# Kernel optimization log

Hardware: AMD Instinct MI355X
Metric: run time of the kernel (lower is better)

## Reference

```python
import jax, jax.numpy as jnp
import numpy as np

BITS = 4
MAXQ = 15          # (1 << BITS) - 1
PACK = 32 // BITS  # 8 values packed per int32


def dequantize(qweight, qzeros, scales, g_idx):
    """GPTQ 4-bit dequant. qweight: [K//8, N] int32, qzeros: [G, N//8] int32,
    scales: [G, N] float, g_idx: [K] int32 -> dense W [K, N] float."""
    N = qweight.shape[1]
    shifts = (jnp.arange(PACK, dtype=jnp.uint32) * BITS)  # [8]
    qw = qweight.astype(jnp.uint32)
    # unpack along K: k = row*8 + j  (matches shifter = (k % 8) * bits)
    w_int = ((qw[:, None, :] >> shifts[None, :, None]) & MAXQ).reshape(-1, N)  # [K, N]
    qz = qzeros.astype(jnp.uint32)
    # unpack along N: n = col*8 + j  (matches zeros_shifter = (n % 8) * bits)
    z_int = ((qz[:, :, None] >> shifts[None, None, :]) & MAXQ).reshape(qzeros.shape[0], -1) + 1  # [G, N]
    dt = scales.dtype
    # group-wise dequant: w = (q - zero) * scale, gathered per-row via g_idx
    return (w_int.astype(dt) - z_int[g_idx].astype(dt)) * scales[g_idx]


def setup_inputs() -> dict:
    key = jax.random.key(0)
    k1, k2, k3, k4, k5 = jax.random.split(key, 5)
    M, K, N, GS = 128, 4096, 11008, 128
    G = K // GS
    x = jax.random.normal(k1, (M, K), dtype=jnp.float32)
    qweight = jax.random.randint(k2, (K // PACK, N), 0, 2147483647, dtype=jnp.int32)
    qzeros = jax.random.randint(k3, (G, N // PACK), 0, 2147483647, dtype=jnp.int32)
    scales = jax.random.uniform(k4, (G, N), dtype=jnp.float32, minval=0.001, maxval=0.01)
    bias = jax.random.normal(k5, (N,), dtype=jnp.float32)
    g_idx = (jnp.arange(K, dtype=jnp.int32) // GS).astype(jnp.int32)
    return {"x": x, "qweight": qweight, "qzeros": qzeros, "scales": scales,
            "bias": bias, "g_idx": g_idx}


def reference(x, qweight, qzeros, scales, bias, g_idx):
    w = dequantize(qweight, qzeros, scales, g_idx)  # [K, N]
    return x @ w + bias
```

## Files before the change

kernel.cpp:

```cpp
#include <hip/hip_runtime.h>
#include <stdint.h>


#define M_DIM 128
#define K_DIM 4096
#define N_DIM 11008
#define GS    128
#define NG    32
#define SPLIT 4
#define GPB   (NG / SPLIT)
#define PART_STRIDE ((size_t)M_DIM * N_DIM)

typedef _Float16 half8  __attribute__((ext_vector_type(8)));
typedef _Float16 half2t __attribute__((ext_vector_type(2)));
typedef _Float16 half4t __attribute__((ext_vector_type(4)));
typedef float    f32x4  __attribute__((ext_vector_type(4)));

__global__ void k_prep(const float* __restrict__ x, const int* __restrict__ qzeros,
                       const float* __restrict__ scales,
                       _Float16* __restrict__ xh, half2t* __restrict__ zsc) {
    int b = blockIdx.x, tid = threadIdx.x;
    if (b < 512) {
        int i = (b * 256 + tid) * 4;
        float4 v = *(const float4*)(x + i);
        half4t o;
        o[0] = (_Float16)v.x; o[1] = (_Float16)v.y;
        o[2] = (_Float16)v.z; o[3] = (_Float16)v.w;
        *(half4t*)(xh + i) = o;
    } else {
        b -= 512;
        int g = b / 43;
        int n = (b - g * 43) * 256 + tid;
        unsigned qz = (unsigned)qzeros[g * (N_DIM / 8) + (n >> 3)];
        float z1 = (float)((qz >> ((n & 7) * 4)) & 15u) + 1.0f;
        float s  = scales[g * N_DIM + n];
        half2t o;
        o[0] = (_Float16)s;
        o[1] = (_Float16)(-z1 * s);
        zsc[g * N_DIM + n] = o;
    }
}

__device__ __forceinline__ void load_lds16(const void* g, void* l) {
    __builtin_amdgcn_global_load_lds(
        (const __attribute__((address_space(1))) unsigned int*)g,
        (__attribute__((address_space(3))) unsigned int*)l, 16, 0, 0);
}

__device__ __forceinline__ half8 dequant8(unsigned q, half2t S2, half2t Z2) {
    const half2t BIAS = __builtin_bit_cast(half2t, 0x64006400u);
    half2t w[4];
#pragma unroll
    for (int p = 0; p < 4; ++p) {
        unsigned r = __builtin_amdgcn_perm(q, q, 0x00010001u * (unsigned)p);
        unsigned t = (r & 0x00F0000Fu) | 0x64006400u;
        w[p] = __builtin_elementwise_fma(__builtin_bit_cast(half2t, t) - BIAS, S2, Z2);
    }
    half4t lo = __builtin_shufflevector(w[0], w[1], 0, 1, 2, 3);
    half4t hi = __builtin_shufflevector(w[2], w[3], 0, 1, 2, 3);
    return __builtin_shufflevector(lo, hi, 0, 1, 2, 3, 4, 5, 6, 7);
}

__global__ __launch_bounds__(512, 4)
void k_gemm(const _Float16* __restrict__ xh,
            const int*      __restrict__ qweight,
            const half2t*   __restrict__ zsc,
            float*          __restrict__ part)
{
    __shared__ _Float16 As[2][128 * 128];

    const int tid  = threadIdx.x;
    const int lane = tid & 63;
    const int w    = tid >> 6;
    const int wx   = w & 1;
    const int wy   = (w >> 1) & 1;
    const int kh   = w >> 2;
    const int q    = lane >> 4;
    const int lr   = lane & 15;

    const int n0 = blockIdx.x * 64;
    const int g0 = blockIdx.y * GPB;
    int ncol[2] = { n0 + wx * 32 + lr, n0 + wx * 32 + lr + 16 };

    f32x4 acc[4][2];
#pragma unroll
    for (int f = 0; f < 4; ++f)
#pragma unroll
        for (int h = 0; h < 2; ++h)
            acc[f][h] = (f32x4){0.f, 0.f, 0.f, 0.f};

    int cm[4], ckb[4];
#pragma unroll
    for (int it = 0; it < 4; ++it) {
        int c = it * 512 + tid;
        cm[it]  = c >> 4;
        ckb[it] = (c & 15) ^ (cm[it] & 15);
    }
    const int wave_lds = w * 64 * 8;

#pragma unroll
    for (int it = 0; it < 4; ++it)
        load_lds16(xh + (size_t)cm[it] * K_DIM + g0 * GS + ckb[it] * 8,
                   &As[0][it * 512 * 8 + wave_lds]);

    unsigned qwA[GPB][4];
    half2t   zs2[GPB][2];
#pragma unroll
    for (int gg = 0; gg < GPB; ++gg) {
        int ga = g0 + gg;
#pragma unroll
        for (int t = 0; t < 2; ++t)
#pragma unroll
            for (int h = 0; h < 2; ++h)
                qwA[gg][t * 2 + h] =
                    (unsigned)qweight[(size_t)(ga * 16 + (kh * 2 + t) * 4 + q) * N_DIM + ncol[h]];
#pragma unroll
        for (int h = 0; h < 2; ++h)
            zs2[gg][h] = zsc[(size_t)ga * N_DIM + ncol[h]];
    }

#pragma unroll
    for (int g = 0; g < GPB; ++g) {
        __syncthreads();

        if (g + 1 < GPB) {
            int gn = g0 + g + 1;
#pragma unroll
            for (int it = 0; it < 4; ++it)
                load_lds16(xh + (size_t)cm[it] * K_DIM + gn * GS + ckb[it] * 8,
                           &As[(g + 1) & 1][it * 512 * 8 + wave_lds]);
        }

        const half2t SC = { (_Float16)1.0f, (_Float16)0.0625f };
        half2t S2[2], Z2[2];
#pragma unroll
        for (int h = 0; h < 2; ++h) {
            half2t ss = __builtin_shufflevector(zs2[g][h], zs2[g][h], 0, 0);
            S2[h] = ss * SC;
            Z2[h] = __builtin_shufflevector(zs2[g][h], zs2[g][h], 1, 1);
        }

#pragma unroll
        for (int t = 0; t < 2; ++t) {
            const int kk = kh * 2 + t;
            half8 bf[2];
#pragma unroll
            for (int h = 0; h < 2; ++h)
                bf[h] = dequant8(qwA[g][t * 2 + h], S2[h], Z2[h]);
#pragma unroll
            for (int f = 0; f < 4; ++f) {
                int m   = wy * 64 + f * 16 + lr;
                int kb2 = (kk * 4 + q) ^ lr;
                half8 af = *(const half8*)(&As[g & 1][m * 128 + kb2 * 8]);
#pragma unroll
                for (int h = 0; h < 2; ++h)
                    acc[f][h] = __builtin_amdgcn_mfma_f32_16x16x32_f16(af, bf[h], acc[f][h], 0, 0, 0);
            }
        }
    }

    __syncthreads();
    float* red = (float*)&As[0][0];
    const int pid = w & 3;
    if (w >= 4) {
#pragma unroll
        for (int f = 0; f < 4; ++f)
#pragma unroll
            for (int h = 0; h < 2; ++h)
                *(f32x4*)(red + pid * 2048 + (f * 2 + h) * 256 + lane * 4) = acc[f][h];
    }
    __syncthreads();
    if (w < 4) {
        float* po = part + (size_t)blockIdx.y * PART_STRIDE;
#pragma unroll
        for (int f = 0; f < 4; ++f) {
            int mrow = wy * 64 + f * 16 + q * 4;
#pragma unroll
            for (int h = 0; h < 2; ++h) {
                f32x4 o = acc[f][h] + *(const f32x4*)(red + pid * 2048 + (f * 2 + h) * 256 + lane * 4);
#pragma unroll
                for (int r = 0; r < 4; ++r)
                    po[(size_t)(mrow + r) * N_DIM + ncol[h]] = o[r];
            }
        }
    }
}

__global__ void k_reduce(const float* __restrict__ part, const float* __restrict__ bias,
                         float* __restrict__ out) {
    int i = (blockIdx.x * 256 + threadIdx.x) * 4;
    int m = i / N_DIM;
    int n = i - m * N_DIM;
    f32x4 s = *(const f32x4*)(bias + n);
#pragma unroll
    for (int sp = 0; sp < SPLIT; ++sp)
        s += *(const f32x4*)(part + sp * PART_STRIDE + i);
    *(f32x4*)(out + i) = s;
}

extern "C" void kernel_launch(void* const* d_in, const int* in_sizes, int n_in,
                              void* d_out, int out_size, void* d_ws, size_t ws_size,
                              hipStream_t stream) {
    const float* x       = (const float*)d_in[0];
    const int*   qweight = (const int*)d_in[1];
    const int*   qzeros  = (const int*)d_in[2];
    const float* scales  = (const float*)d_in[3];
    const float* bias    = (const float*)d_in[4];

    char* ws = (char*)d_ws;
    _Float16* xh   = (_Float16*)ws;
    half2t*   zsc  = (half2t*)(ws + 1048576);
    float*    part = (float*)(ws + 1048576 + 1409024);

    k_prep  <<<dim3(1888),            dim3(256), 0, stream>>>(x, qzeros, scales, xh, zsc);
    k_gemm  <<<dim3(N_DIM/64, SPLIT), dim3(512), 0, stream>>>(xh, qweight, zsc, part);
    k_reduce<<<dim3(1376),            dim3(256), 0, stream>>>(part, bias, (float*)d_out);
}
```

Before: 105.2 us.

## Replace split-K with M-split tiling and fuse bias into GEMM epilogue

Replaces the split-K decomposition, which wrote four fp32 partial outputs and needed a separate reduce kernel, with full-K accumulation per block. The block now covers 64 rows of M, using a 256-wide K tile with a register-prefetched weight pipeline. Bias is added in the epilogue and the reduce launch plus the partial-buffer traffic are removed. The trade-off is that each weight tile is now read and dequantized twice, once per M half, and each block runs a longer serial K loop (16 iterations) with less per-block MFMA reuse of the dequantized B fragments.

```diff
diff --git a/kernel.cpp b/kernel.cpp
--- a/kernel.cpp
+++ b/kernel.cpp
@@ -6,10 +6,8 @@
 #define K_DIM 4096
 #define N_DIM 11008
 #define GS    128
-#define NG    32
-#define SPLIT 4
-#define GPB   (NG / SPLIT)
-#define PART_STRIDE ((size_t)M_DIM * N_DIM)
+#define BK    256
+#define NITER (K_DIM / BK)
 
 typedef _Float16 half8  __attribute__((ext_vector_type(8)));
 typedef _Float16 half2t __attribute__((ext_vector_type(2)));
@@ -65,9 +63,10 @@
 void k_gemm(const _Float16* __restrict__ xh,
             const int*      __restrict__ qweight,
             const half2t*   __restrict__ zsc,
-            float*          __restrict__ part)
+            const float*    __restrict__ bias,
+            float*          __restrict__ out)
 {
-    __shared__ _Float16 As[2][128 * 128];
+    __shared__ _Float16 As[2][64 * 256];
 
     const int tid  = threadIdx.x;
     const int lane = tid & 63;
@@ -79,12 +78,12 @@
     const int lr   = lane & 15;
 
     const int n0 = blockIdx.x * 64;
-    const int g0 = blockIdx.y * GPB;
+    const int m0 = blockIdx.y * 64;
     int ncol[2] = { n0 + wx * 32 + lr, n0 + wx * 32 + lr + 16 };
 
-    f32x4 acc[4][2];
-#pragma unroll
-    for (int f = 0; f < 4; ++f)
+    f32x4 acc[2][2];
+#pragma unroll
+    for (int f = 0; f < 2; ++f)
 #pragma unroll
         for (int h = 0; h < 2; ++h)
             acc[f][h] = (f32x4){0.f, 0.f, 0.f, 0.f};
@@ -93,65 +92,75 @@
 #pragma unroll
     for (int it = 0; it < 4; ++it) {
         int c = it * 512 + tid;
-        cm[it]  = c >> 4;
-        ckb[it] = (c & 15) ^ (cm[it] & 15);
-    }
-    const int wave_lds = w * 64 * 8;
+        cm[it] = c >> 5;
+        int j  = c & 31;
+        ckb[it] = (j & 16) | ((j & 15) ^ (cm[it] & 15));
+    }
+    const int wave_lds = w * 512;
 
 #pragma unroll
     for (int it = 0; it < 4; ++it)
-        load_lds16(xh + (size_t)cm[it] * K_DIM + g0 * GS + ckb[it] * 8,
-                   &As[0][it * 512 * 8 + wave_lds]);
-
-    unsigned qwA[GPB][4];
-    half2t   zs2[GPB][2];
-#pragma unroll
-    for (int gg = 0; gg < GPB; ++gg) {
-        int ga = g0 + gg;
-#pragma unroll
-        for (int t = 0; t < 2; ++t)
+        load_lds16(xh + (size_t)(m0 + cm[it]) * K_DIM + ckb[it] * 8,
+                   &As[0][it * 4096 + wave_lds]);
+    unsigned qwn[8];
+    half2t   zsn[2];
+#pragma unroll
+    for (int t = 0; t < 4; ++t)
+#pragma unroll
+        for (int h = 0; h < 2; ++h)
+            qwn[t * 2 + h] = (unsigned)qweight[(size_t)((kh * 4 + t) * 4 + q) * N_DIM + ncol[h]];
+#pragma unroll
+    for (int h = 0; h < 2; ++h) zsn[h] = zsc[(size_t)kh * N_DIM + ncol[h]];
+    float bv[2] = { bias[ncol[0]], bias[ncol[1]] };
+
+#pragma unroll 2
+    for (int i = 0; i < NITER; ++i) {
+        unsigned qw[8];
+        half2t   zs[2];
+#pragma unroll
+        for (int j = 0; j < 8; ++j) qw[j] = qwn[j];
+#pragma unroll
+        for (int h = 0; h < 2; ++h) zs[h] = zsn[h];
+
+        __syncthreads();
+
+        if (i + 1 < NITER) {
+#pragma unroll
+            for (int it = 0; it < 4; ++it)
+                load_lds16(xh + (size_t)(m0 + cm[it]) * K_DIM + (i + 1) * BK + ckb[it] * 8,
+                           &As[(i + 1) & 1][it * 4096 + wave_lds]);
+#pragma unroll
+            for (int t = 0; t < 4; ++t)
+#pragma unroll
+                for (int h = 0; h < 2; ++h)
+                    qwn[t * 2 + h] = (unsigned)qweight[(size_t)((i + 1) * 32 + (kh * 4 + t) * 4 + q) * N_DIM + ncol[h]];
 #pragma unroll
             for (int h = 0; h < 2; ++h)
-                qwA[gg][t * 2 + h] =
-                    (unsigned)qweight[(size_t)(ga * 16 + (kh * 2 + t) * 4 + q) * N_DIM + ncol[h]];
-#pragma unroll
-        for (int h = 0; h < 2; ++h)
-            zs2[gg][h] = zsc[(size_t)ga * N_DIM + ncol[h]];
-    }
-
-#pragma unroll
-    for (int g = 0; g < GPB; ++g) {
-        __syncthreads();
-
-        if (g + 1 < GPB) {
-            int gn = g0 + g + 1;
-#pragma unroll
-            for (int it = 0; it < 4; ++it)
-                load_lds16(xh + (size_t)cm[it] * K_DIM + gn * GS + ckb[it] * 8,
-                           &As[(g + 1) & 1][it * 512 * 8 + wave_lds]);
+                zsn[h] = zsc[(size_t)(2 * (i + 1) + kh) * N_DIM + ncol[h]];
         }
 
         const half2t SC = { (_Float16)1.0f, (_Float16)0.0625f };
         half2t S2[2], Z2[2];
 #pragma unroll
         for (int h = 0; h < 2; ++h) {
-            half2t ss = __builtin_shufflevector(zs2[g][h], zs2[g][h], 0, 0);
+            half2t ss = __builtin_shufflevector(zs[h], zs[h], 0, 0);
             S2[h] = ss * SC;
-            Z2[h] = __builtin_shufflevector(zs2[g][h], zs2[g][h], 1, 1);
-        }
-
-#pragma unroll
-        for (int t = 0; t < 2; ++t) {
-            const int kk = kh * 2 + t;
+            Z2[h] = __builtin_shufflevector(zs[h], zs[h], 1, 1);
+        }
+
+#pragma unroll
+        for (int t = 0; t < 4; ++t) {
+            const int kk = kh * 4 + t;
             half8 bf[2];
 #pragma unroll
             for (int h = 0; h < 2; ++h)
-                bf[h] = dequant8(qwA[g][t * 2 + h], S2[h], Z2[h]);
-#pragma unroll
-            for (int f = 0; f < 4; ++f) {
-                int m   = wy * 64 + f * 16 + lr;
-                int kb2 = (kk * 4 + q) ^ lr;
-                half8 af = *(const half8*)(&As[g & 1][m * 128 + kb2 * 8]);
+                bf[h] = dequant8(qw[t * 2 + h], S2[h], Z2[h]);
+#pragma unroll
+            for (int f = 0; f < 2; ++f) {
+                int m    = wy * 32 + f * 16 + lr;
+                int kb2  = kk * 4 + q;
+                int phys = (kb2 & 16) | ((kb2 & 15) ^ lr);
+                half8 af = *(const half8*)(&As[i & 1][m * 256 + phys * 8]);
 #pragma unroll
                 for (int h = 0; h < 2; ++h)
                     acc[f][h] = __builtin_amdgcn_mfma_f32_16x16x32_f16(af, bf[h], acc[f][h], 0, 0, 0);
@@ -162,40 +171,27 @@
     __syncthreads();
     float* red = (float*)&As[0][0];
     const int pid = w & 3;
-    if (w >= 4) {
-#pragma unroll
-        for (int f = 0; f < 4; ++f)
+    if (kh == 1) {
+#pragma unroll
+        for (int f = 0; f < 2; ++f)
 #pragma unroll
             for (int h = 0; h < 2; ++h)
                 *(f32x4*)(red + pid * 2048 + (f * 2 + h) * 256 + lane * 4) = acc[f][h];
     }
     __syncthreads();
-    if (w < 4) {
-        float* po = part + (size_t)blockIdx.y * PART_STRIDE;
-#pragma unroll
-        for (int f = 0; f < 4; ++f) {
-            int mrow = wy * 64 + f * 16 + q * 4;
+    if (kh == 0) {
+#pragma unroll
+        for (int f = 0; f < 2; ++f) {
+            int mrow = m0 + wy * 32 + f * 16 + q * 4;
 #pragma unroll
             for (int h = 0; h < 2; ++h) {
                 f32x4 o = acc[f][h] + *(const f32x4*)(red + pid * 2048 + (f * 2 + h) * 256 + lane * 4);
 #pragma unroll
                 for (int r = 0; r < 4; ++r)
-                    po[(size_t)(mrow + r) * N_DIM + ncol[h]] = o[r];
+                    out[(size_t)(mrow + r) * N_DIM + ncol[h]] = o[r] + bv[h];
             }
         }
     }
-}
-
-__global__ void k_reduce(const float* __restrict__ part, const float* __restrict__ bias,
-                         float* __restrict__ out) {
-    int i = (blockIdx.x * 256 + threadIdx.x) * 4;
-    int m = i / N_DIM;
-    int n = i - m * N_DIM;
-    f32x4 s = *(const f32x4*)(bias + n);
-#pragma unroll
-    for (int sp = 0; sp < SPLIT; ++sp)
-        s += *(const f32x4*)(part + sp * PART_STRIDE + i);
-    *(f32x4*)(out + i) = s;
 }
 
 extern "C" void kernel_launch(void* const* d_in, const int* in_sizes, int n_in,
@@ -208,11 +204,9 @@
     const float* bias    = (const float*)d_in[4];
 
     char* ws = (char*)d_ws;
-    _Float16* xh   = (_Float16*)ws;
-    half2t*   zsc  = (half2t*)(ws + 1048576);
-    float*    part = (float*)(ws + 1048576 + 1409024);
-
-    k_prep  <<<dim3(1888),            dim3(256), 0, stream>>>(x, qzeros, scales, xh, zsc);
-    k_gemm  <<<dim3(N_DIM/64, SPLIT), dim3(512), 0, stream>>>(xh, qweight, zsc, part);
-    k_reduce<<<dim3(1376),            dim3(256), 0, stream>>>(part, bias, (float*)d_out);
-}
+    _Float16* xh  = (_Float16*)ws;
+    half2t*   zsc = (half2t*)(ws + 1048576);
+
+    k_prep<<<dim3(1888),    dim3(256), 0, stream>>>(x, qzeros, scales, xh, zsc);
+    k_gemm<<<dim3(172, 2),  dim3(512), 0, stream>>>(xh, qweight, zsc, bias, (float*)d_out);
+}
```

After: 112.7 us. 7.1% more time.

## Pre-swizzle activations into MFMA fragment layout and drop LDS staging

Applied to the files above, without the earlier changes.

The prep kernel now writes the fp16 activations already arranged in per-lane MFMA A-fragment order. The GEMM kernel can then load A fragments straight from global memory with register double-buffering instead of staging tiles through LDS with barriers. Blocks shrink to 256 threads, and each wave owns 32 rows across the full 64 columns and the whole split-K range, which removes the in-block LDS reduction. The cost is that A fragments are re-read from global/L2 by every block, with no LDS reuse across waves, and weight loads are pipelined one step ahead rather than fully prefetched.

```diff
diff --git a/kernel.cpp b/kernel.cpp
--- a/kernel.cpp
+++ b/kernel.cpp
@@ -6,31 +6,39 @@
 #define K_DIM 4096
 #define N_DIM 11008
 #define GS    128
-#define NG    32
 #define SPLIT 4
-#define GPB   (NG / SPLIT)
+#define STEPS 32
 #define PART_STRIDE ((size_t)M_DIM * N_DIM)
 
 typedef _Float16 half8  __attribute__((ext_vector_type(8)));
+typedef _Float16 half4t __attribute__((ext_vector_type(4)));
 typedef _Float16 half2t __attribute__((ext_vector_type(2)));
-typedef _Float16 half4t __attribute__((ext_vector_type(4)));
 typedef float    f32x4  __attribute__((ext_vector_type(4)));
 
 __global__ void k_prep(const float* __restrict__ x, const int* __restrict__ qzeros,
                        const float* __restrict__ scales,
-                       _Float16* __restrict__ xh, half2t* __restrict__ zsc) {
-    int b = blockIdx.x, tid = threadIdx.x;
-    if (b < 512) {
-        int i = (b * 256 + tid) * 4;
-        float4 v = *(const float4*)(x + i);
-        half4t o;
-        o[0] = (_Float16)v.x; o[1] = (_Float16)v.y;
-        o[2] = (_Float16)v.z; o[3] = (_Float16)v.w;
-        *(half4t*)(xh + i) = o;
+                       _Float16* __restrict__ xf, half2t* __restrict__ zsc) {
+    int b = blockIdx.x, t = threadIdx.x;
+    if (b < 256) {
+        int slot = b * 256 + t;
+        int lane = slot & 63;
+        int pair = slot >> 6;
+        int mt = pair >> 7, kb = pair & 127;
+        int row = mt * 16 + (lane & 15);
+        int col = kb * 32 + (lane >> 4) * 8;
+        const float* px = x + (size_t)row * K_DIM + col;
+        float4 v0 = *(const float4*)px;
+        float4 v1 = *(const float4*)(px + 4);
+        half8 o;
+        o[0] = (_Float16)v0.x; o[1] = (_Float16)v0.y;
+        o[2] = (_Float16)v0.z; o[3] = (_Float16)v0.w;
+        o[4] = (_Float16)v1.x; o[5] = (_Float16)v1.y;
+        o[6] = (_Float16)v1.z; o[7] = (_Float16)v1.w;
+        *(half8*)(xf + (size_t)slot * 8) = o;
     } else {
-        b -= 512;
+        b -= 256;
         int g = b / 43;
-        int n = (b - g * 43) * 256 + tid;
+        int n = (b - g * 43) * 256 + t;
         unsigned qz = (unsigned)qzeros[g * (N_DIM / 8) + (n >> 3)];
         float z1 = (float)((qz >> ((n & 7) * 4)) & 15u) + 1.0f;
         float s  = scales[g * N_DIM + n];
@@ -39,12 +47,6 @@
         o[1] = (_Float16)(-z1 * s);
         zsc[g * N_DIM + n] = o;
     }
-}
-
-__device__ __forceinline__ void load_lds16(const void* g, void* l) {
-    __builtin_amdgcn_global_load_lds(
-        (const __attribute__((address_space(1))) unsigned int*)g,
-        (__attribute__((address_space(3))) unsigned int*)l, 16, 0, 0);
 }
 
 __device__ __forceinline__ half8 dequant8(unsigned q, half2t S2, half2t Z2) {
@@ -56,133 +58,107 @@
         unsigned t = (r & 0x00F0000Fu) | 0x64006400u;
         w[p] = __builtin_elementwise_fma(__builtin_bit_cast(half2t, t) - BIAS, S2, Z2);
     }
-    half4t lo = __builtin_shufflevector(w[0], w[1], 0, 1, 2, 3);
-    half4t hi = __builtin_shufflevector(w[2], w[3], 0, 1, 2, 3);
-    return __builtin_shufflevector(lo, hi, 0, 1, 2, 3, 4, 5, 6, 7);
+    half4t w01 = __builtin_shufflevector(w[0], w[1], 0, 1, 2, 3);
+    half4t w23 = __builtin_shufflevector(w[2], w[3], 0, 1, 2, 3);
+    return __builtin_shufflevector(w01, w23, 0, 1, 2, 3, 4, 5, 6, 7);
 }
 
-__global__ __launch_bounds__(512, 4)
-void k_gemm(const _Float16* __restrict__ xh,
+__global__ __launch_bounds__(256, 4)
+void k_gemm(const _Float16* __restrict__ xf,
             const int*      __restrict__ qweight,
             const half2t*   __restrict__ zsc,
             float*          __restrict__ part)
 {
-    __shared__ _Float16 As[2][128 * 128];
-
     const int tid  = threadIdx.x;
     const int lane = tid & 63;
     const int w    = tid >> 6;
-    const int wx   = w & 1;
-    const int wy   = (w >> 1) & 1;
-    const int kh   = w >> 2;
     const int q    = lane >> 4;
     const int lr   = lane & 15;
 
     const int n0 = blockIdx.x * 64;
-    const int g0 = blockIdx.y * GPB;
-    int ncol[2] = { n0 + wx * 32 + lr, n0 + wx * 32 + lr + 16 };
+    const int by = blockIdx.y;
 
-    f32x4 acc[4][2];
+    int ncol[4];
 #pragma unroll
-    for (int f = 0; f < 4; ++f)
+    for (int j = 0; j < 4; ++j) ncol[j] = n0 + j * 16 + lr;
+
+    f32x4 acc[2][4];
 #pragma unroll
-        for (int h = 0; h < 2; ++h)
-            acc[f][h] = (f32x4){0.f, 0.f, 0.f, 0.f};
+    for (int f = 0; f < 2; ++f)
+#pragma unroll
+        for (int j = 0; j < 4; ++j)
+            acc[f][j] = (f32x4){0.f, 0.f, 0.f, 0.f};
 
-    int cm[4], ckb[4];
+    const _Float16* pa0 = xf + (((size_t)(2 * w) * 128 + by * 32) << 9) + lane * 8;
+    const _Float16* pa1 = pa0 + ((size_t)128 << 9);
+    const int* pq = qweight + (size_t)(by * 128 + q) * N_DIM;
+    const half2t* pz = zsc + (size_t)(by * 8) * N_DIM;
+
+    half8 a0 = *(const half8*)pa0;
+    half8 a1 = *(const half8*)pa1;
+    unsigned qc[4];
+    half2t   zc[4];
 #pragma unroll
-    for (int it = 0; it < 4; ++it) {
-        int c = it * 512 + tid;
-        cm[it]  = c >> 4;
-        ckb[it] = (c & 15) ^ (cm[it] & 15);
-    }
-    const int wave_lds = w * 64 * 8;
-
-#pragma unroll
-    for (int it = 0; it < 4; ++it)
-        load_lds16(xh + (size_t)cm[it] * K_DIM + g0 * GS + ckb[it] * 8,
-                   &As[0][it * 512 * 8 + wave_lds]);
-
-    unsigned qwA[GPB][4];
-    half2t   zs2[GPB][2];
-#pragma unroll
-    for (int gg = 0; gg < GPB; ++gg) {
-        int ga = g0 + gg;
-#pragma unroll
-        for (int t = 0; t < 2; ++t)
-#pragma unroll
-            for (int h = 0; h < 2; ++h)
-                qwA[gg][t * 2 + h] =
-                    (unsigned)qweight[(size_t)(ga * 16 + (kh * 2 + t) * 4 + q) * N_DIM + ncol[h]];
-#pragma unroll
-        for (int h = 0; h < 2; ++h)
-            zs2[gg][h] = zsc[(size_t)ga * N_DIM + ncol[h]];
+    for (int j = 0; j < 4; ++j) {
+        qc[j] = (unsigned)pq[ncol[j]];
+        zc[j] = pz[ncol[j]];
     }
 
+    for (int g = 0; g < 8; ++g) {
+        const half2t SC = { (_Float16)1.0f, (_Float16)0.0625f };
+        half2t S2[4], Z2[4];
 #pragma unroll
-    for (int g = 0; g < GPB; ++g) {
-        __syncthreads();
-
-        if (g + 1 < GPB) {
-            int gn = g0 + g + 1;
-#pragma unroll
-            for (int it = 0; it < 4; ++it)
-                load_lds16(xh + (size_t)cm[it] * K_DIM + gn * GS + ckb[it] * 8,
-                           &As[(g + 1) & 1][it * 512 * 8 + wave_lds]);
-        }
-
-        const half2t SC = { (_Float16)1.0f, (_Float16)0.0625f };
-        half2t S2[2], Z2[2];
-#pragma unroll
-        for (int h = 0; h < 2; ++h) {
-            half2t ss = __builtin_shufflevector(zs2[g][h], zs2[g][h], 0, 0);
-            S2[h] = ss * SC;
-            Z2[h] = __builtin_shufflevector(zs2[g][h], zs2[g][h], 1, 1);
+        for (int j = 0; j < 4; ++j) {
+            half2t ss = __builtin_shufflevector(zc[j], zc[j], 0, 0);
+            S2[j] = ss * SC;
+            Z2[j] = __builtin_shufflevector(zc[j], zc[j], 1, 1);
         }
 
 #pragma unroll
-        for (int t = 0; t < 2; ++t) {
-            const int kk = kh * 2 + t;
-            half8 bf[2];
+        for (int t = 0; t < 4; ++t) {
+            const int s  = g * 4 + t;
+            const int sn = (s + 1 < STEPS) ? s + 1 : s;
+
+            half8 na0 = *(const half8*)(pa0 + (size_t)sn * 512);
+            half8 na1 = *(const half8*)(pa1 + (size_t)sn * 512);
+            unsigned nq[4];
 #pragma unroll
-            for (int h = 0; h < 2; ++h)
-                bf[h] = dequant8(qwA[g][t * 2 + h], S2[h], Z2[h]);
+            for (int j = 0; j < 4; ++j)
+                nq[j] = (unsigned)pq[(size_t)sn * 4 * N_DIM + ncol[j]];
+            half2t nz[4];
+            if (t == 3) {
+                int gn = (g + 1 < 8) ? g + 1 : g;
 #pragma unroll
-            for (int f = 0; f < 4; ++f) {
-                int m   = wy * 64 + f * 16 + lr;
-                int kb2 = (kk * 4 + q) ^ lr;
-                half8 af = *(const half8*)(&As[g & 1][m * 128 + kb2 * 8]);
+                for (int j = 0; j < 4; ++j)
+                    nz[j] = pz[(size_t)gn * N_DIM + ncol[j]];
+            }
+
 #pragma unroll
-                for (int h = 0; h < 2; ++h)
-                    acc[f][h] = __builtin_amdgcn_mfma_f32_16x16x32_f16(af, bf[h], acc[f][h], 0, 0, 0);
+            for (int j = 0; j < 4; ++j) {
+                half8 bf = dequant8(qc[j], S2[j], Z2[j]);
+                acc[0][j] = __builtin_amdgcn_mfma_f32_16x16x32_f16(a0, bf, acc[0][j], 0, 0, 0);
+                acc[1][j] = __builtin_amdgcn_mfma_f32_16x16x32_f16(a1, bf, acc[1][j], 0, 0, 0);
+            }
+
+            a0 = na0; a1 = na1;
+#pragma unroll
+            for (int j = 0; j < 4; ++j) qc[j] = nq[j];
+            if (t == 3) {
+#pragma unroll
+                for (int j = 0; j < 4; ++j) zc[j] = nz[j];
             }
         }
     }
 
-    __syncthreads();
-    float* red = (float*)&As[0][0];
-    const int pid = w & 3;
-    if (w >= 4) {
+    float* po = part + (size_t)by * PART_STRIDE;
 #pragma unroll
-        for (int f = 0; f < 4; ++f)
+    for (int f = 0; f < 2; ++f) {
+        int mrow = w * 32 + f * 16 + q * 4;
 #pragma unroll
-            for (int h = 0; h < 2; ++h)
-                *(f32x4*)(red + pid * 2048 + (f * 2 + h) * 256 + lane * 4) = acc[f][h];
-    }
-    __syncthreads();
-    if (w < 4) {
-        float* po = part + (size_t)blockIdx.y * PART_STRIDE;
+        for (int j = 0; j < 4; ++j)
 #pragma unroll
-        for (int f = 0; f < 4; ++f) {
-            int mrow = wy * 64 + f * 16 + q * 4;
-#pragma unroll
-            for (int h = 0; h < 2; ++h) {
-                f32x4 o = acc[f][h] + *(const f32x4*)(red + pid * 2048 + (f * 2 + h) * 256 + lane * 4);
-#pragma unroll
-                for (int r = 0; r < 4; ++r)
-                    po[(size_t)(mrow + r) * N_DIM + ncol[h]] = o[r];
-            }
-        }
+            for (int r = 0; r < 4; ++r)
+                po[(size_t)(mrow + r) * N_DIM + ncol[j]] = acc[f][j][r];
     }
 }
 
@@ -208,11 +184,11 @@
     const float* bias    = (const float*)d_in[4];
 
     char* ws = (char*)d_ws;
-    _Float16* xh   = (_Float16*)ws;
+    _Float16* xf   = (_Float16*)ws;
     half2t*   zsc  = (half2t*)(ws + 1048576);
     float*    part = (float*)(ws + 1048576 + 1409024);
 
-    k_prep  <<<dim3(1888),            dim3(256), 0, stream>>>(x, qzeros, scales, xh, zsc);
-    k_gemm  <<<dim3(N_DIM/64, SPLIT), dim3(512), 0, stream>>>(xh, qweight, zsc, part);
+    k_prep  <<<dim3(1632),            dim3(256), 0, stream>>>(x, qzeros, scales, xf, zsc);
+    k_gemm  <<<dim3(N_DIM/64, SPLIT), dim3(256), 0, stream>>>(xf, qweight, zsc, part);
     k_reduce<<<dim3(1376),            dim3(256), 0, stream>>>(part, bias, (float*)d_out);
 }
```

New measurement: 110.3 us. 4.8% more time.
